# Performance work log

Measured on AMD Instinct MI355X. Metric: run time of the kernel, lower is better.

Reference implementation:

```python
import jax, jax.numpy as jnp
import numpy as np

N_NODES = 50000
N_EDGES = 800000
D = 128          # embedding_dim
G = 3            # group_size
K = 4            # window_size
ALPHA = -0.5
WEIGHTS = (1.0, 1.0, 7.81, 45.28)
EPS = 1e-12      # torch F.normalize clamp_min


def _striped_projection(key):
    """Striped sparse random projection, densified (matches torch coalesce+to_dense)."""
    num_groups = D // G  # 42; columns 126..127 remain zero, as in the original
    k_off, k_sign = jax.random.split(key)
    row_idx = jnp.repeat(jnp.arange(N_NODES), num_groups)
    base = jnp.tile(jnp.arange(0, num_groups * G, G), N_NODES)
    off = jax.random.randint(k_off, (N_NODES * num_groups,), 0, G)
    col_idx = base + off
    scale = float(np.sqrt(G))  # 1/sqrt(density), density = 1/g
    vals = (jax.random.randint(k_sign, (N_NODES * num_groups,), 0, 2).astype(jnp.float32) * 2.0 - 1.0) * scale
    return jnp.zeros((N_NODES, D), jnp.float32).at[row_idx, col_idx].add(vals)


def setup_inputs() -> dict:
    key = jax.random.key(0)
    k1, k2, k3 = jax.random.split(key, 3)
    edge_row = jax.random.randint(k1, (N_EDGES,), 0, N_NODES)
    edge_col = jax.random.randint(k2, (N_EDGES,), 0, N_NODES)
    edge_val = jnp.ones((N_EDGES,), jnp.float32)
    R = _striped_projection(k3)
    return {"edge_row": edge_row, "edge_col": edge_col, "edge_val": edge_val, "R": R}


def reference(edge_row, edge_col, edge_val, R):
    N = R.shape[0]
    # degrees = row sums of sparse adjacency; zeros -> 1
    deg = jax.ops.segment_sum(edge_val, edge_row, num_segments=N)
    deg = jnp.where(deg == 0, 1.0, deg)
    # initial degree scaling: N_curr = R * deg**alpha
    x = R * (deg ** ALPHA)[:, None]
    inv_deg = (1.0 / deg)[:, None]
    acc = jnp.zeros_like(R)
    for i in range(K):
        # SpMM: out[r] = sum_{e: row[e]==r} val[e] * x[col[e]]
        x = jax.ops.segment_sum(edge_val[:, None] * x[edge_col], edge_row, num_segments=N)
        x = x * inv_deg  # transition-matrix ('trans') scaling
        nrm = jnp.maximum(jnp.sqrt(jnp.sum(x * x, axis=1, keepdims=True)), EPS)
        acc = acc + (x / nrm) * WEIGHTS[i]
    mean = acc.mean(axis=0)
    std = jnp.std(acc, axis=0, ddof=1)  # torch .std() is unbiased
    std = jnp.where(std == 0, 1.0, std)
    return (acc - mean) / std
```

## Files before the change

### kernel.cpp

```cpp
#include <hip/hip_runtime.h>
#include <math.h>

#define NN 50000
#define NE 800000
#define DD 128
#define NBKT 256
#define RPB 196
#define BCAP 3840
#define CHUNK 2048
#define NCHUNK ((NE + CHUNK - 1) / CHUNK)
#define SPMM_NBLK (NN / 16)

static __device__ __forceinline__ float blo(unsigned int p) { return __uint_as_float(p << 16); }
static __device__ __forceinline__ float bhi(unsigned int p) { return __uint_as_float(p & 0xffff0000u); }
static __device__ __forceinline__ unsigned int pack2bf(float a, float b) {
    unsigned int ua = __float_as_uint(a);
    unsigned int ub = __float_as_uint(b);
    ua = ua + 0x7FFFu + ((ua >> 16) & 1u);
    ub = ub + 0x7FFFu + ((ub >> 16) & 1u);
    return (ua >> 16) | (ub & 0xffff0000u);
}

static __global__ __launch_bounds__(512) void bin_kernel(
    const int* __restrict__ erow, const int* __restrict__ ecol, const float* __restrict__ eval_,
    int* __restrict__ bucket_cursor, uint2* __restrict__ binned) {
    __shared__ uint2 sorted[CHUNK];
    __shared__ unsigned char sbin[CHUNK];
    __shared__ int hist[NBKT];
    __shared__ int bstart[NBKT];
    __shared__ int bcur[NBKT];
    __shared__ int gbase[NBKT];
    __shared__ int tmp[NBKT];

    int t = threadIdx.x;
    int cbase = blockIdx.x * CHUNK;
    int cn = NE - cbase; if (cn > CHUNK) cn = CHUNK;

    for (int i = t; i < NBKT; i += 512) hist[i] = 0;
    __syncthreads();

    unsigned int rc[4]; unsigned int vv[4]; int bb[4];
    int nloc = 0;
    for (int i = t; i < cn; i += 512) {
        int g = cbase + i;
        int r = erow[g];
        int c = ecol[g];
        float v = eval_[g];
        rc[nloc] = (unsigned)r | ((unsigned)c << 16);
        vv[nloc] = __float_as_uint(v);
        int b = r / RPB;
        bb[nloc] = b;
        atomicAdd(&hist[b], 1);
        ++nloc;
    }
    __syncthreads();

    int hv = (t < NBKT) ? hist[t] : 0;
    if (t < NBKT) tmp[t] = hv;
    __syncthreads();
    for (int off = 1; off < NBKT; off <<= 1) {
        int u = (t < NBKT && t >= off) ? tmp[t - off] : 0;
        __syncthreads();
        if (t < NBKT) tmp[t] += u;
        __syncthreads();
    }
    if (t < NBKT) {
        int ex = tmp[t] - hv;
        bstart[t] = ex;
        bcur[t] = ex;
        gbase[t] = atomicAdd(&bucket_cursor[t], hv);
    }
    __syncthreads();

    for (int k = 0; k < nloc; ++k) {
        int pos = atomicAdd(&bcur[bb[k]], 1);
        sorted[pos] = make_uint2(rc[k], vv[k]);
        sbin[pos] = (unsigned char)bb[k];
    }
    __syncthreads();

    for (int i = t; i < cn; i += 512) {
        int b = sbin[i];
        binned[(size_t)b * BCAP + gbase[b] + (i - bstart[b])] = sorted[i];
    }
}

static __global__ __launch_bounds__(512) void sort_kernel(
    const uint2* __restrict__ binned, const int* __restrict__ bucket_cursor,
    uint2* __restrict__ csr, int* __restrict__ row_start, float* __restrict__ deg) {
    __shared__ uint2 buf[BCAP];
    __shared__ int hist[RPB];
    __shared__ int rcur[RPB];
    __shared__ float fdeg[RPB];
    __shared__ int pscan[NBKT];
    int b = blockIdx.x;
    int t = threadIdx.x;
    int lo = b * RPB;

    int pv = (t < NBKT) ? bucket_cursor[t] : 0;
    if (t < NBKT) pscan[t] = pv;
    if (t < RPB) { hist[t] = 0; fdeg[t] = 0.0f; }
    __syncthreads();
    for (int off = 1; off < NBKT; off <<= 1) {
        int u = (t < NBKT && t >= off) ? pscan[t - off] : 0;
        __syncthreads();
        if (t < NBKT) pscan[t] += u;
        __syncthreads();
    }
    int gb = (b == 0) ? 0 : pscan[b - 1];
    int cnt = pscan[b] - gb;

    for (int i = t; i < cnt; i += 512) {
        uint2 e = binned[(size_t)b * BCAP + i];
        buf[i] = e;
        int rr = (int)(e.x & 0xFFFFu) - lo;
        atomicAdd(&hist[rr], 1);
        atomicAdd(&fdeg[rr], __uint_as_float(e.y));
    }
    __syncthreads();
    int hv = (t < RPB) ? hist[t] : 0;
    if (t < RPB) rcur[t] = hv;
    __syncthreads();
    for (int off = 1; off < RPB; off <<= 1) {
        int u = (t < RPB && t >= off) ? rcur[t - off] : 0;
        __syncthreads();
        if (t < RPB) rcur[t] += u;
        __syncthreads();
    }
    if (t < RPB) {
        int excl = rcur[t] - hv;
        int r = lo + t;
        if (r < NN) {
            row_start[r] = gb + excl;
            float d = fdeg[t];
            deg[r] = (d == 0.0f) ? 1.0f : d;
        }
        rcur[t] = excl;
    }
    if (b == NBKT - 1 && t == 0) row_start[NN] = gb + cnt;
    __syncthreads();
    for (int i = t; i < cnt; i += 512) {
        uint2 e = buf[i];
        int rr = (int)(e.x & 0xFFFFu) - lo;
        int pos = atomicAdd(&rcur[rr], 1);
        csr[(size_t)gb + pos] = make_uint2(e.x >> 16, e.y);
    }
}

static __global__ __launch_bounds__(256) void x0_kernel(
    const float* __restrict__ R, const float* __restrict__ deg, uint4* __restrict__ x0) {
    int idx = blockIdx.x * 256 + threadIdx.x;
    int row = idx >> 4;
    float sc = rsqrtf(deg[row]);
    const float4* __restrict__ R4 = (const float4*)R;
    float4 f0 = R4[(size_t)idx * 2];
    float4 f1 = R4[(size_t)idx * 2 + 1];
    x0[idx] = make_uint4(pack2bf(f0.x * sc, f0.y * sc), pack2bf(f0.z * sc, f0.w * sc),
                         pack2bf(f1.x * sc, f1.y * sc), pack2bf(f1.z * sc, f1.w * sc));
}

static __global__ __launch_bounds__(256) void spmm_fused_kernel(
    const int* __restrict__ row_start, const uint2* __restrict__ csr,
    const uint4* __restrict__ x4, const float* __restrict__ deg,
    uint4* __restrict__ x_next4, float* __restrict__ s_out, float weight) {
    int wave = threadIdx.x >> 6;
    int lane = threadIdx.x & 63;
    int quarter = lane >> 4;
    int sub = lane & 15;
    int row = blockIdx.x * 16 + wave * 4 + quarter;
    int s = row_start[row];
    int e = row_start[row + 1];

    float a0 = 0.f, a1 = 0.f, a2 = 0.f, a3 = 0.f, a4 = 0.f, a5 = 0.f, a6 = 0.f, a7 = 0.f;
    for (int base = s; base < e; base += 16) {
        int j = base + sub;
        int cl = 0;
        float vl = 0.0f;
        if (j < e) { uint2 t2 = csr[j]; cl = (int)t2.x; vl = __uint_as_float(t2.y); }
        int cnt = e - base; if (cnt > 16) cnt = 16;
        for (int k = 0; k < cnt; k += 4) {
            int l0 = quarter * 16 + k;
            int c0 = __shfl(cl, l0);
            int c1 = __shfl(cl, l0 + 1);
            int c2 = __shfl(cl, l0 + 2);
            int c3 = __shfl(cl, l0 + 3);
            float v0 = __shfl(vl, l0);
            float v1 = __shfl(vl, l0 + 1);
            float v2 = __shfl(vl, l0 + 2);
            float v3 = __shfl(vl, l0 + 3);
            uint4 p0 = x4[(size_t)c0 * 16 + sub];
            uint4 p1 = x4[(size_t)c1 * 16 + sub];
            uint4 p2 = x4[(size_t)c2 * 16 + sub];
            uint4 p3 = x4[(size_t)c3 * 16 + sub];
            a0 += v0 * blo(p0.x); a1 += v0 * bhi(p0.x); a2 += v0 * blo(p0.y); a3 += v0 * bhi(p0.y);
            a4 += v0 * blo(p0.z); a5 += v0 * bhi(p0.z); a6 += v0 * blo(p0.w); a7 += v0 * bhi(p0.w);
            a0 += v1 * blo(p1.x); a1 += v1 * bhi(p1.x); a2 += v1 * blo(p1.y); a3 += v1 * bhi(p1.y);
            a4 += v1 * blo(p1.z); a5 += v1 * bhi(p1.z); a6 += v1 * blo(p1.w); a7 += v1 * bhi(p1.w);
            a0 += v2 * blo(p2.x); a1 += v2 * bhi(p2.x); a2 += v2 * blo(p2.y); a3 += v2 * bhi(p2.y);
            a4 += v2 * blo(p2.z); a5 += v2 * bhi(p2.z); a6 += v2 * blo(p2.w); a7 += v2 * bhi(p2.w);
            a0 += v3 * blo(p3.x); a1 += v3 * bhi(p3.x); a2 += v3 * blo(p3.y); a3 += v3 * bhi(p3.y);
            a4 += v3 * blo(p3.z); a5 += v3 * bhi(p3.z); a6 += v3 * blo(p3.w); a7 += v3 * bhi(p3.w);
        }
    }

    float id = 1.0f / deg[row];
    a0 *= id; a1 *= id; a2 *= id; a3 *= id; a4 *= id; a5 *= id; a6 *= id; a7 *= id;

    float ss = a0 * a0 + a1 * a1 + a2 * a2 + a3 * a3 + a4 * a4 + a5 * a5 + a6 * a6 + a7 * a7;
#pragma unroll
    for (int m = 1; m <= 8; m <<= 1) ss += __shfl_xor(ss, m);
    float nrm = fmaxf(sqrtf(ss), 1e-12f);

    x_next4[(size_t)row * 16 + sub] = make_uint4(pack2bf(a0, a1), pack2bf(a2, a3),
                                                 pack2bf(a4, a5), pack2bf(a6, a7));
    if (sub == 0) s_out[row] = weight / nrm;
}

static __global__ __launch_bounds__(256) void spmm_last_kernel(
    const int* __restrict__ row_start, const uint2* __restrict__ csr,
    const uint4* __restrict__ xin, const float* __restrict__ deg,
    const uint4* __restrict__ x1, const uint4* __restrict__ x2, const uint4* __restrict__ x3,
    const float* __restrict__ s1, const float* __restrict__ s2, const float* __restrict__ s3,
    float* __restrict__ out, float* __restrict__ psum, float* __restrict__ psumsq, float weight) {
    __shared__ float shs[256 * 8];
    __shared__ float shq[256 * 8];
    int wave = threadIdx.x >> 6;
    int lane = threadIdx.x & 63;
    int quarter = lane >> 4;
    int sub = lane & 15;
    int row = blockIdx.x * 16 + wave * 4 + quarter;
    int s = row_start[row];
    int e = row_start[row + 1];

    float a0 = 0.f, a1 = 0.f, a2 = 0.f, a3 = 0.f, a4 = 0.f, a5 = 0.f, a6 = 0.f, a7 = 0.f;
    for (int base = s; base < e; base += 16) {
        int j = base + sub;
        int cl = 0;
        float vl = 0.0f;
        if (j < e) { uint2 t2 = csr[j]; cl = (int)t2.x; vl = __uint_as_float(t2.y); }
        int cnt = e - base; if (cnt > 16) cnt = 16;
        for (int k = 0; k < cnt; k += 4) {
            int l0 = quarter * 16 + k;
            int c0 = __shfl(cl, l0);
            int c1 = __shfl(cl, l0 + 1);
            int c2 = __shfl(cl, l0 + 2);
            int c3 = __shfl(cl, l0 + 3);
            float v0 = __shfl(vl, l0);
            float v1 = __shfl(vl, l0 + 1);
            float v2 = __shfl(vl, l0 + 2);
            float v3 = __shfl(vl, l0 + 3);
            uint4 p0 = xin[(size_t)c0 * 16 + sub];
            uint4 p1 = xin[(size_t)c1 * 16 + sub];
            uint4 p2 = xin[(size_t)c2 * 16 + sub];
            uint4 p3 = xin[(size_t)c3 * 16 + sub];
            a0 += v0 * blo(p0.x); a1 += v0 * bhi(p0.x); a2 += v0 * blo(p0.y); a3 += v0 * bhi(p0.y);
            a4 += v0 * blo(p0.z); a5 += v0 * bhi(p0.z); a6 += v0 * blo(p0.w); a7 += v0 * bhi(p0.w);
            a0 += v1 * blo(p1.x); a1 += v1 * bhi(p1.x); a2 += v1 * blo(p1.y); a3 += v1 * bhi(p1.y);
            a4 += v1 * blo(p1.z); a5 += v1 * bhi(p1.z); a6 += v1 * blo(p1.w); a7 += v1 * bhi(p1.w);
            a0 += v2 * blo(p2.x); a1 += v2 * bhi(p2.x); a2 += v2 * blo(p2.y); a3 += v2 * bhi(p2.y);
            a4 += v2 * blo(p2.z); a5 += v2 * bhi(p2.z); a6 += v2 * blo(p2.w); a7 += v2 * bhi(p2.w);
            a0 += v3 * blo(p3.x); a1 += v3 * bhi(p3.x); a2 += v3 * blo(p3.y); a3 += v3 * bhi(p3.y);
            a4 += v3 * blo(p3.z); a5 += v3 * bhi(p3.z); a6 += v3 * blo(p3.w); a7 += v3 * bhi(p3.w);
        }
    }

    float id = 1.0f / deg[row];
    a0 *= id; a1 *= id; a2 *= id; a3 *= id; a4 *= id; a5 *= id; a6 *= id; a7 *= id;

    float ss = a0 * a0 + a1 * a1 + a2 * a2 + a3 * a3 + a4 * a4 + a5 * a5 + a6 * a6 + a7 * a7;
#pragma unroll
    for (int m = 1; m <= 8; m <<= 1) ss += __shfl_xor(ss, m);
    float nrm = fmaxf(sqrtf(ss), 1e-12f);
    float w4 = weight / nrm;

    size_t xi = (size_t)row * 16 + sub;
    float w1 = s1[row], w2 = s2[row], w3 = s3[row];
    uint4 q1 = x1[xi], q2 = x2[xi], q3 = x3[xi];
    float v[8];
    v[0] = w1 * blo(q1.x) + w2 * blo(q2.x) + w3 * blo(q3.x) + w4 * a0;
    v[1] = w1 * bhi(q1.x) + w2 * bhi(q2.x) + w3 * bhi(q3.x) + w4 * a1;
    v[2] = w1 * blo(q1.y) + w2 * blo(q2.y) + w3 * blo(q3.y) + w4 * a2;
    v[3] = w1 * bhi(q1.y) + w2 * bhi(q2.y) + w3 * bhi(q3.y) + w4 * a3;
    v[4] = w1 * blo(q1.z) + w2 * blo(q2.z) + w3 * blo(q3.z) + w4 * a4;
    v[5] = w1 * bhi(q1.z) + w2 * bhi(q2.z) + w3 * bhi(q3.z) + w4 * a5;
    v[6] = w1 * blo(q1.w) + w2 * blo(q2.w) + w3 * blo(q3.w) + w4 * a6;
    v[7] = w1 * bhi(q1.w) + w2 * bhi(q2.w) + w3 * bhi(q3.w) + w4 * a7;

    float4* out4 = (float4*)out;
    out4[(size_t)row * 32 + sub * 2]     = make_float4(v[0], v[1], v[2], v[3]);
    out4[(size_t)row * 32 + sub * 2 + 1] = make_float4(v[4], v[5], v[6], v[7]);

    int t = threadIdx.x;
#pragma unroll
    for (int j = 0; j < 8; ++j) {
        shs[t * 8 + j] = v[j];
        shq[t * 8 + j] = v[j] * v[j];
    }
    __syncthreads();
    if (t < DD) {
        int cs = t >> 3, cj = t & 7;
        float sacc = 0.0f, qacc = 0.0f;
        for (int g = 0; g < 16; ++g) {
            int src = (g * 16 + cs) * 8 + cj;
            sacc += shs[src];
            qacc += shq[src];
        }
        psum[(size_t)blockIdx.x * DD + t] = sacc;
        psumsq[(size_t)blockIdx.x * DD + t] = qacc;
    }
}

static __global__ __launch_bounds__(256) void fold_kernel(
    const float* __restrict__ psum, const float* __restrict__ psumsq,
    float* __restrict__ mean, float* __restrict__ invstd) {
    __shared__ double ss[256], qq[256];
    int c = blockIdx.x;
    int t = threadIdx.x;
    double s = 0.0, q = 0.0;
    for (int b = t; b < SPMM_NBLK; b += 256) {
        s += (double)psum[(size_t)b * DD + c];
        q += (double)psumsq[(size_t)b * DD + c];
    }
    ss[t] = s; qq[t] = q;
    __syncthreads();
    for (int off = 128; off > 0; off >>= 1) {
        if (t < off) { ss[t] += ss[t + off]; qq[t] += qq[t + off]; }
        __syncthreads();
    }
    if (t == 0) {
        double m = ss[0] / (double)NN;
        double var = (qq[0] - (double)NN * m * m) / (double)(NN - 1);
        if (var < 0.0) var = 0.0;
        double sd = sqrt(var);
        if (sd == 0.0) sd = 1.0;
        mean[c] = (float)m;
        invstd[c] = (float)(1.0 / sd);
    }
}

static __global__ __launch_bounds__(256) void normalize_kernel(
    float* __restrict__ out, const float* __restrict__ mean, const float* __restrict__ invstd) {
    int i = blockIdx.x * blockDim.x + threadIdx.x;
    int c4 = i & 31;
    float4 m = ((const float4*)mean)[c4];
    float4 is = ((const float4*)invstd)[c4];
    float4* out4 = (float4*)out;
    float4 v = out4[i];
    v.x = (v.x - m.x) * is.x;
    v.y = (v.y - m.y) * is.y;
    v.z = (v.z - m.z) * is.z;
    v.w = (v.w - m.w) * is.w;
    out4[i] = v;
}

extern "C" void kernel_launch(void* const* d_in, const int* in_sizes, int n_in,
                              void* d_out, int out_size, void* d_ws, size_t ws_size,
                              hipStream_t stream) {
    const int* erow = (const int*)d_in[0];
    const int* ecol = (const int*)d_in[1];
    const float* eval_ = (const float*)d_in[2];
    const float* R = (const float*)d_in[3];
    float* out = (float*)d_out;

    char* ws = (char*)d_ws;
    size_t off = 0;
    auto alloc = [&](size_t bytes) -> char* {
        char* p = ws + off;
        off += (bytes + 255) & ~(size_t)255;
        return p;
    };
    float* deg          = (float*)alloc(NN * sizeof(float));
    int* bucket_cursor  = (int*)alloc(NBKT * sizeof(int));
    int* row_start      = (int*)alloc((NN + 1) * sizeof(int));
    uint2* binned       = (uint2*)alloc((size_t)NBKT * BCAP * sizeof(uint2));
    uint2* csr          = (uint2*)alloc((size_t)NE * sizeof(uint2));
    uint4* x0           = (uint4*)alloc((size_t)NN * 16 * sizeof(uint4));
    uint4* x1           = (uint4*)alloc((size_t)NN * 16 * sizeof(uint4));
    uint4* x2           = (uint4*)alloc((size_t)NN * 16 * sizeof(uint4));
    uint4* x3           = (uint4*)alloc((size_t)NN * 16 * sizeof(uint4));
    float* s1           = (float*)alloc(NN * sizeof(float));
    float* s2           = (float*)alloc(NN * sizeof(float));
    float* s3           = (float*)alloc(NN * sizeof(float));
    float* psum         = (float*)alloc((size_t)SPMM_NBLK * DD * sizeof(float));
    float* psumsq       = (float*)alloc((size_t)SPMM_NBLK * DD * sizeof(float));
    float* meanbuf      = (float*)alloc(DD * sizeof(float));
    float* invstdb      = (float*)alloc(DD * sizeof(float));

    hipMemsetAsync(bucket_cursor, 0, NBKT * sizeof(int), stream);

    bin_kernel<<<NCHUNK, 512, 0, stream>>>(erow, ecol, eval_, bucket_cursor, binned);
    sort_kernel<<<NBKT, 512, 0, stream>>>(binned, bucket_cursor, csr, row_start, deg);
    x0_kernel<<<SPMM_NBLK, 256, 0, stream>>>(R, deg, x0);

    spmm_fused_kernel<<<SPMM_NBLK, 256, 0, stream>>>(row_start, csr, x0, deg, x1, s1, 1.0f);
    spmm_fused_kernel<<<SPMM_NBLK, 256, 0, stream>>>(row_start, csr, x1, deg, x2, s2, 1.0f);
    spmm_fused_kernel<<<SPMM_NBLK, 256, 0, stream>>>(row_start, csr, x2, deg, x3, s3, 7.81f);
    spmm_last_kernel<<<SPMM_NBLK, 256, 0, stream>>>(row_start, csr, x3, deg, x1, x2, x3,
                                                    s1, s2, s3, out, psum, psumsq, 45.28f);

    fold_kernel<<<DD, 256, 0, stream>>>(psum, psumsq, meanbuf, invstdb);
    normalize_kernel<<<NN * 32 / 256, 256, 0, stream>>>(out, meanbuf, invstdb);
}
```

Baseline: 247.6 us.

## Compress sign-only projection rows to 2-bit codes for first SpMM gather

The prep kernel checks whether each projection row has only zeros and entries of one common magnitude. If so, it encodes each row as 2-bit sign codes plus one scale. The first SpMM then gathers these compact codes instead of full bf16 rows, cutting gather traffic for that pass, at the cost of extra decode arithmetic. A global flag, set by atomics, switches back to the original bf16 gather whenever any row breaks the pattern, which adds an extra buffer write in the prep kernel.

```diff
diff --git a/kernel.cpp b/kernel.cpp
--- a/kernel.cpp
+++ b/kernel.cpp
@@ -147,16 +147,147 @@
     }
 }
 
-static __global__ __launch_bounds__(256) void x0_kernel(
-    const float* __restrict__ R, const float* __restrict__ deg, uint4* __restrict__ x0) {
+static __global__ __launch_bounds__(256) void pk_kernel(
+    const float* __restrict__ R, const float* __restrict__ deg,
+    uint4* __restrict__ x0, unsigned int* __restrict__ pks, int* __restrict__ flag) {
     int idx = blockIdx.x * 256 + threadIdx.x;
-    int row = idx >> 4;
-    float sc = rsqrtf(deg[row]);
+    int node = idx >> 4;
+    int sub = idx & 15;
+    float sc = rsqrtf(deg[node]);
     const float4* __restrict__ R4 = (const float4*)R;
     float4 f0 = R4[(size_t)idx * 2];
     float4 f1 = R4[(size_t)idx * 2 + 1];
     x0[idx] = make_uint4(pack2bf(f0.x * sc, f0.y * sc), pack2bf(f0.z * sc, f0.w * sc),
                          pack2bf(f1.x * sc, f1.y * sc), pack2bf(f1.z * sc, f1.w * sc));
+
+    float v[8] = {f0.x, f0.y, f0.z, f0.w, f1.x, f1.y, f1.z, f1.w};
+    float am = 0.0f;
+#pragma unroll
+    for (int j = 0; j < 8; ++j) am = fmaxf(am, fabsf(v[j]));
+#pragma unroll
+    for (int m = 1; m < 16; m <<= 1) am = fmaxf(am, __shfl_xor(am, m));
+
+    bool viol = false;
+    unsigned int code16 = 0;
+#pragma unroll
+    for (int j = 0; j < 8; ++j) {
+        float x = v[j];
+        unsigned int code = (x == 0.0f) ? 0u : ((x < 0.0f) ? 3u : 1u);
+        if (x != 0.0f && fabsf(x) != am) viol = true;
+        code16 |= code << (2 * j);
+    }
+    unsigned int other = __shfl_xor(code16, 1);
+    unsigned int word = (sub & 1) ? ((code16 << 16) | other) : (code16 | (other << 16));
+    if (!(sub & 1)) pks[(size_t)node * 16 + (sub >> 1)] = word;
+    if (sub == 0) pks[(size_t)node * 16 + 8] = __float_as_uint(am * sc);
+    if (viol) atomicOr(flag, 1);
+}
+
+static __global__ __launch_bounds__(256) void spmm_first_kernel(
+    const int* __restrict__ row_start, const uint2* __restrict__ csr,
+    const unsigned int* __restrict__ pks, const uint4* __restrict__ x4,
+    const float* __restrict__ deg, const int* __restrict__ flag,
+    uint4* __restrict__ x_next4, float* __restrict__ s_out, float weight) {
+    int wave = threadIdx.x >> 6;
+    int lane = threadIdx.x & 63;
+    int quarter = lane >> 4;
+    int sub = lane & 15;
+    int row = blockIdx.x * 16 + wave * 4 + quarter;
+    int s = row_start[row];
+    int e = row_start[row + 1];
+
+    float a[8] = {0.f, 0.f, 0.f, 0.f, 0.f, 0.f, 0.f, 0.f};
+
+    if (*flag == 0) {
+        size_t wofs = (size_t)(sub >> 1);
+        int hsh = (sub & 1) * 16;
+        for (int base = s; base < e; base += 16) {
+            int j = base + sub;
+            int cl = 0;
+            float vl = 0.0f;
+            if (j < e) { uint2 t2 = csr[j]; cl = (int)t2.x; vl = __uint_as_float(t2.y); }
+            int cnt = e - base; if (cnt > 16) cnt = 16;
+            for (int k = 0; k < cnt; k += 4) {
+                int l0 = quarter * 16 + k;
+                int c0 = __shfl(cl, l0);
+                int c1 = __shfl(cl, l0 + 1);
+                int c2 = __shfl(cl, l0 + 2);
+                int c3 = __shfl(cl, l0 + 3);
+                float v0 = __shfl(vl, l0);
+                float v1 = __shfl(vl, l0 + 1);
+                float v2 = __shfl(vl, l0 + 2);
+                float v3 = __shfl(vl, l0 + 3);
+                unsigned int w0 = pks[(size_t)c0 * 16 + wofs];
+                unsigned int w1 = pks[(size_t)c1 * 16 + wofs];
+                unsigned int w2 = pks[(size_t)c2 * 16 + wofs];
+                unsigned int w3 = pks[(size_t)c3 * 16 + wofs];
+                float u0 = v0 * __uint_as_float(pks[(size_t)c0 * 16 + 8]);
+                float u1 = v1 * __uint_as_float(pks[(size_t)c1 * 16 + 8]);
+                float u2 = v2 * __uint_as_float(pks[(size_t)c2 * 16 + 8]);
+                float u3 = v3 * __uint_as_float(pks[(size_t)c3 * 16 + 8]);
+                unsigned int h0 = (w0 >> hsh) & 0xFFFFu;
+                unsigned int h1 = (w1 >> hsh) & 0xFFFFu;
+                unsigned int h2 = (w2 >> hsh) & 0xFFFFu;
+                unsigned int h3 = (w3 >> hsh) & 0xFFFFu;
+#pragma unroll
+                for (int jj = 0; jj < 8; ++jj) {
+                    int d0 = (int)((h0 >> (2 * jj)) & 3u);
+                    int d1 = (int)((h1 >> (2 * jj)) & 3u);
+                    int d2 = (int)((h2 >> (2 * jj)) & 3u);
+                    int d3 = (int)((h3 >> (2 * jj)) & 3u);
+                    a[jj] += u0 * (float)((d0 & 1) - (d0 & 2));
+                    a[jj] += u1 * (float)((d1 & 1) - (d1 & 2));
+                    a[jj] += u2 * (float)((d2 & 1) - (d2 & 2));
+                    a[jj] += u3 * (float)((d3 & 1) - (d3 & 2));
+                }
+            }
+        }
+    } else {
+        for (int base = s; base < e; base += 16) {
+            int j = base + sub;
+            int cl = 0;
+            float vl = 0.0f;
+            if (j < e) { uint2 t2 = csr[j]; cl = (int)t2.x; vl = __uint_as_float(t2.y); }
+            int cnt = e - base; if (cnt > 16) cnt = 16;
+            for (int k = 0; k < cnt; k += 4) {
+                int l0 = quarter * 16 + k;
+                int c0 = __shfl(cl, l0);
+                int c1 = __shfl(cl, l0 + 1);
+                int c2 = __shfl(cl, l0 + 2);
+                int c3 = __shfl(cl, l0 + 3);
+                float v0 = __shfl(vl, l0);
+                float v1 = __shfl(vl, l0 + 1);
+                float v2 = __shfl(vl, l0 + 2);
+                float v3 = __shfl(vl, l0 + 3);
+                uint4 p0 = x4[(size_t)c0 * 16 + sub];
+                uint4 p1 = x4[(size_t)c1 * 16 + sub];
+                uint4 p2 = x4[(size_t)c2 * 16 + sub];
+                uint4 p3 = x4[(size_t)c3 * 16 + sub];
+                a[0] += v0 * blo(p0.x); a[1] += v0 * bhi(p0.x); a[2] += v0 * blo(p0.y); a[3] += v0 * bhi(p0.y);
+                a[4] += v0 * blo(p0.z); a[5] += v0 * bhi(p0.z); a[6] += v0 * blo(p0.w); a[7] += v0 * bhi(p0.w);
+                a[0] += v1 * blo(p1.x); a[1] += v1 * bhi(p1.x); a[2] += v1 * blo(p1.y); a[3] += v1 * bhi(p1.y);
+                a[4] += v1 * blo(p1.z); a[5] += v1 * bhi(p1.z); a[6] += v1 * blo(p1.w); a[7] += v1 * bhi(p1.w);
+                a[0] += v2 * blo(p2.x); a[1] += v2 * bhi(p2.x); a[2] += v2 * blo(p2.y); a[3] += v2 * bhi(p2.y);
+                a[4] += v2 * blo(p2.z); a[5] += v2 * bhi(p2.z); a[6] += v2 * blo(p2.w); a[7] += v2 * bhi(p2.w);
+                a[0] += v3 * blo(p3.x); a[1] += v3 * bhi(p3.x); a[2] += v3 * blo(p3.y); a[3] += v3 * bhi(p3.y);
+                a[4] += v3 * blo(p3.z); a[5] += v3 * bhi(p3.z); a[6] += v3 * blo(p3.w); a[7] += v3 * bhi(p3.w);
+            }
+        }
+    }
+
+    float id = 1.0f / deg[row];
+#pragma unroll
+    for (int jj = 0; jj < 8; ++jj) a[jj] *= id;
+
+    float ss = a[0]*a[0] + a[1]*a[1] + a[2]*a[2] + a[3]*a[3]
+             + a[4]*a[4] + a[5]*a[5] + a[6]*a[6] + a[7]*a[7];
+#pragma unroll
+    for (int m = 1; m <= 8; m <<= 1) ss += __shfl_xor(ss, m);
+    float nrm = fmaxf(sqrtf(ss), 1e-12f);
+
+    x_next4[(size_t)row * 16 + sub] = make_uint4(pack2bf(a[0], a[1]), pack2bf(a[2], a[3]),
+                                                 pack2bf(a[4], a[5]), pack2bf(a[6], a[7]));
+    if (sub == 0) s_out[row] = weight / nrm;
 }
 
 static __global__ __launch_bounds__(256) void spmm_fused_kernel(
@@ -370,7 +501,7 @@
         return p;
     };
     float* deg          = (float*)alloc(NN * sizeof(float));
-    int* bucket_cursor  = (int*)alloc(NBKT * sizeof(int));
+    int* bucket_cursor  = (int*)alloc((NBKT + 1) * sizeof(int));
     int* row_start      = (int*)alloc((NN + 1) * sizeof(int));
     uint2* binned       = (uint2*)alloc((size_t)NBKT * BCAP * sizeof(uint2));
     uint2* csr          = (uint2*)alloc((size_t)NE * sizeof(uint2));
@@ -378,6 +509,7 @@
     uint4* x1           = (uint4*)alloc((size_t)NN * 16 * sizeof(uint4));
     uint4* x2           = (uint4*)alloc((size_t)NN * 16 * sizeof(uint4));
     uint4* x3           = (uint4*)alloc((size_t)NN * 16 * sizeof(uint4));
+    unsigned int* pks   = (unsigned int*)alloc((size_t)NN * 16 * sizeof(unsigned int));
     float* s1           = (float*)alloc(NN * sizeof(float));
     float* s2           = (float*)alloc(NN * sizeof(float));
     float* s3           = (float*)alloc(NN * sizeof(float));
@@ -385,14 +517,16 @@
     float* psumsq       = (float*)alloc((size_t)SPMM_NBLK * DD * sizeof(float));
     float* meanbuf      = (float*)alloc(DD * sizeof(float));
     float* invstdb      = (float*)alloc(DD * sizeof(float));
-
-    hipMemsetAsync(bucket_cursor, 0, NBKT * sizeof(int), stream);
+    int* sflag          = &bucket_cursor[NBKT];
+
+    hipMemsetAsync(bucket_cursor, 0, (NBKT + 1) * sizeof(int), stream);
 
     bin_kernel<<<NCHUNK, 512, 0, stream>>>(erow, ecol, eval_, bucket_cursor, binned);
     sort_kernel<<<NBKT, 512, 0, stream>>>(binned, bucket_cursor, csr, row_start, deg);
-    x0_kernel<<<SPMM_NBLK, 256, 0, stream>>>(R, deg, x0);
-
-    spmm_fused_kernel<<<SPMM_NBLK, 256, 0, stream>>>(row_start, csr, x0, deg, x1, s1, 1.0f);
+    pk_kernel<<<SPMM_NBLK, 256, 0, stream>>>(R, deg, x0, pks, sflag);
+
+    spmm_first_kernel<<<SPMM_NBLK, 256, 0, stream>>>(row_start, csr, pks, x0, deg, sflag,
+                                                     x1, s1, 1.0f);
     spmm_fused_kernel<<<SPMM_NBLK, 256, 0, stream>>>(row_start, csr, x1, deg, x2, s2, 1.0f);
     spmm_fused_kernel<<<SPMM_NBLK, 256, 0, stream>>>(row_start, csr, x2, deg, x3, s3, 7.81f);
     spmm_last_kernel<<<SPMM_NBLK, 256, 0, stream>>>(row_start, csr, x3, deg, x1, x2, x3,
```

Result: slower. 254.3 us (+2.7%).
